# Optimization experiments

Measured on AMD Instinct MI355X. Metric: run time of the kernel, lower is better.

The kernel has to match this reference:

```python
import jax, jax.numpy as jnp
import numpy as np

# init config (from module __init__ / docstring example)
VOXEL_SIZE = np.array([0.2, 0.2, 8.0], dtype=np.float32)
PC_RANGE = np.array([0.0, -25.6, -3.0, 51.2, 25.6, 5.0], dtype=np.float32)
MAX_PTS = 32
MAX_VOX = 16000
GRID = (int((PC_RANGE[3] - PC_RANGE[0]) / VOXEL_SIZE[0]),
        int((PC_RANGE[4] - PC_RANGE[1]) / VOXEL_SIZE[1]),
        int((PC_RANGE[5] - PC_RANGE[2]) / VOXEL_SIZE[2]))  # (256, 256, 1)

N_POINTS = 4_000_000
C_FEAT = 4  # xyz + intensity


def setup_inputs() -> dict:
    key = jax.random.key(0)
    u = jax.random.uniform(key, (N_POINTS, C_FEAT), dtype=jnp.float32)
    lo = jnp.array([PC_RANGE[0], PC_RANGE[1], PC_RANGE[2], 0.0], jnp.float32)
    span = jnp.array([PC_RANGE[3] - PC_RANGE[0], PC_RANGE[4] - PC_RANGE[1],
                      PC_RANGE[5] - PC_RANGE[2], 1.0], jnp.float32)
    points = u * span + lo  # uniformly inside the point-cloud range
    return {"points": points}


def reference(points):
    """Hard voxelization. Returns fixed-size (padded) outputs:
    voxels [MAX_VOX, MAX_PTS, C], coords [MAX_VOX, 3] int32, num_points [MAX_VOX] int32.
    Unused voxel slots are zero (num_points==0), matching torch semantics up to padding."""
    N, C = points.shape
    Gx, Gy, Gz = GRID
    lo = jnp.asarray(PC_RANGE[:3])
    hi = jnp.asarray(PC_RANGE[3:])
    vsz = jnp.asarray(VOXEL_SIZE)

    xyz = points[:, :3]
    valid = jnp.all((xyz >= lo) & (xyz < hi), axis=1)  # in-range mask

    coords = jnp.floor((xyz - lo) / vsz).astype(jnp.int32)
    coords = jnp.clip(coords, 0, jnp.array([Gx - 1, Gy - 1, Gz - 1], jnp.int32))

    # linear voxel hash; invalid points get sentinel so they sort to the end
    BIG = Gx * Gy * Gz
    vhash = coords[:, 0] * (Gy * Gz) + coords[:, 1] * Gz + coords[:, 2]
    vhash = jnp.where(valid, vhash, BIG)

    order = jnp.argsort(vhash)
    sh = vhash[order]          # [N] sorted hashes
    sc = coords[order]         # [N,3]
    sp = points[order]         # [N,C]
    svalid = sh < BIG

    # segment boundaries of the sorted hash stream (== torch.unique inverse groups)
    newv = jnp.concatenate([jnp.array([True]), sh[1:] != sh[:-1]]) & svalid
    vid = jnp.cumsum(newv.astype(jnp.int32)) - 1   # voxel id per point (sorted order)

    idx = jnp.arange(N, dtype=jnp.int32)
    start = jax.lax.cummax(jnp.where(newv, idx, 0))  # index of first point of own voxel
    rank = idx - start                                # position within voxel

    keep = svalid & (rank < MAX_PTS) & (vid < MAX_VOX)
    vid_s = jnp.where(keep, vid, MAX_VOX)   # route dropped points to dump row
    rank_s = jnp.where(keep, rank, 0)

    voxels = jnp.zeros((MAX_VOX + 1, MAX_PTS, C), points.dtype)
    voxels = voxels.at[vid_s, rank_s].set(sp)[:MAX_VOX]

    cvid = jnp.where(newv & (vid < MAX_VOX), vid, MAX_VOX)
    coords_out = jnp.zeros((MAX_VOX + 1, 3), jnp.int32).at[cvid].set(sc)[:MAX_VOX]

    num_points = jax.ops.segment_sum(keep.astype(jnp.int32), vid_s,
                                     num_segments=MAX_VOX + 1)[:MAX_VOX]
    return voxels, coords_out, num_points
```

## Files before the change

### kernel.cpp

```cpp
#include <hip/hip_runtime.h>

#define NBINS    65536
#define NWORDS   16384
#define MAXVOX   16000
#define MAXPTS   32
#define NBLK     256
#define RSEG     8

#define COORDS_OFF (MAXVOX * MAXPTS * 4)
#define NP_OFF     (COORDS_OFF + MAXVOX * 3)

#define OFF_COUNTS   0u
#define OFF_STARTS   (256u << 10)
#define OFF_BINOF    (512u << 10)
#define OFF_PARTC    (576u << 10)
#define OFF_PARTO    (577u << 10)
#define OFF_VBIT     (640u << 10)
#define OFF_BINS16   (2u << 20)
#define OFF_PARTIAL  (10u << 20)
#define OFF_MEMBERS  (26u << 20)

__global__ __launch_bounds__(1024) void k_hist(const float4* __restrict__ pts, int n,
                                               unsigned short* __restrict__ bins16,
                                               unsigned long long* __restrict__ vbit,
                                               unsigned* __restrict__ partial) {
    __shared__ unsigned sh[NWORDS];
    int t = threadIdx.x, b = blockIdx.x;
    for (int w = t; w < NWORDS; w += 1024) sh[w] = 0u;
    __syncthreads();

    int chunk = (n + NBLK - 1) / NBLK;
    int s = b * chunk;
    int e = min(n, s + chunk);
    int k = 0;
    for (int i = s + t; i < e; i += 1024, ++k) {
        float4 p = pts[i];
        bool valid = (p.x >= 0.0f)   & (p.x < 51.2f) &
                     (p.y >= -25.6f) & (p.y < 25.6f) &
                     (p.z >= -3.0f)  & (p.z < 5.0f);
        int cx = (int)floorf((p.x - 0.0f)  / 0.2f);
        int cy = (int)floorf((p.y + 25.6f) / 0.2f);
        int cz = (int)floorf((p.z + 3.0f)  / 8.0f);
        cx = min(max(cx, 0), 255);
        cy = min(max(cy, 0), 255);
        cz = min(max(cz, 0), 0);
        unsigned bin = (unsigned)(cx * 256 + cy + cz);
        bins16[i] = (unsigned short)bin;
        unsigned long long mask = __ballot(valid);
        if ((t & 63) == 0) vbit[(size_t)b * 256 + (t >> 6) + k * 16] = mask;
        if (valid) atomicAdd(&sh[bin >> 2], 1u << ((bin & 3u) * 8u));
    }
    __syncthreads();
    unsigned* myp = partial + (size_t)b * NWORDS;
    for (int w = t; w < NWORDS; w += 1024) myp[w] = sh[w];
}

__global__ __launch_bounds__(512) void k_reduce(unsigned* __restrict__ partial,
                                                unsigned* __restrict__ counts,
                                                unsigned* __restrict__ partC,
                                                unsigned* __restrict__ partO,
                                                unsigned* __restrict__ binof) {
    __shared__ unsigned cache[NBLK][64];
    __shared__ unsigned segsum[RSEG][64][4];
    __shared__ unsigned red[512];
    int t = threadIdx.x;
    int g = blockIdx.x * 512 + t;
    if (g < MAXVOX) binof[g] = 0xFFFFFFFFu;

    int wl  = t & 63;
    int seg = t >> 6;
    int w   = blockIdx.x * 64 + wl;
    int blk0 = seg * (NBLK / RSEG);

    unsigned a0 = 0, a1 = 0, a2 = 0, a3 = 0;
    for (int b = 0; b < NBLK / RSEG; ++b) {
        unsigned v = partial[(size_t)(blk0 + b) * NWORDS + w];
        cache[blk0 + b][wl] = v;
        a0 += v & 255u; a1 += (v >> 8) & 255u;
        a2 += (v >> 16) & 255u; a3 += (v >> 24) & 255u;
    }
    segsum[seg][wl][0] = a0; segsum[seg][wl][1] = a1;
    segsum[seg][wl][2] = a2; segsum[seg][wl][3] = a3;
    __syncthreads();

    unsigned b0 = 0, b1 = 0, b2 = 0, b3 = 0;
    for (int s2 = 0; s2 < seg; ++s2) {
        b0 += segsum[s2][wl][0]; b1 += segsum[s2][wl][1];
        b2 += segsum[s2][wl][2]; b3 += segsum[s2][wl][3];
    }
    for (int b = 0; b < NBLK / RSEG; ++b) {
        unsigned v = cache[blk0 + b][wl];
        partial[(size_t)(blk0 + b) * NWORDS + w] =
            b0 | (b1 << 8) | (b2 << 16) | (b3 << 24);
        b0 += v & 255u; b1 += (v >> 8) & 255u;
        b2 += (v >> 16) & 255u; b3 += (v >> 24) & 255u;
    }

    unsigned mySum = 0, myOcc = 0;
    if (seg == RSEG - 1) {
        counts[w * 4 + 0] = b0; counts[w * 4 + 1] = b1;
        counts[w * 4 + 2] = b2; counts[w * 4 + 3] = b3;
        mySum = b0 + b1 + b2 + b3;
        myOcc = (b0 > 0u) + (b1 > 0u) + (b2 > 0u) + (b3 > 0u);
    }
    red[t] = mySum; __syncthreads();
    for (int off = 256; off > 0; off >>= 1) { if (t < off) red[t] += red[t + off]; __syncthreads(); }
    if (t == 0) partC[blockIdx.x] = red[0];
    __syncthreads();
    red[t] = myOcc; __syncthreads();
    for (int off = 256; off > 0; off >>= 1) { if (t < off) red[t] += red[t + off]; __syncthreads(); }
    if (t == 0) partO[blockIdx.x] = red[0];
}

__global__ __launch_bounds__(256) void k_scan3(const unsigned* __restrict__ counts,
                                               const unsigned* __restrict__ partC,
                                               const unsigned* __restrict__ partO,
                                               unsigned* __restrict__ starts,
                                               unsigned* __restrict__ binof,
                                               float* __restrict__ out) {
    __shared__ unsigned rc[256], ro[256], sc[256], so[256];
    int t = threadIdx.x;
    int bin = blockIdx.x * 256 + t;
    unsigned c = counts[bin];
    unsigned occ = (c > 0u) ? 1u : 0u;

    rc[t] = (t < blockIdx.x) ? partC[t] : 0u;
    ro[t] = (t < blockIdx.x) ? partO[t] : 0u;
    sc[t] = c; so[t] = occ;
    __syncthreads();
    for (int off = 128; off > 0; off >>= 1) {
        if (t < off) { rc[t] += rc[t + off]; ro[t] += ro[t + off]; }
        __syncthreads();
    }
    unsigned baseC = rc[0], baseO = ro[0];
    for (int off = 1; off < 256; off <<= 1) {
        unsigned ac = (t >= off) ? sc[t - off] : 0u;
        unsigned ao = (t >= off) ? so[t - off] : 0u;
        __syncthreads();
        sc[t] += ac; so[t] += ao;
        __syncthreads();
    }
    unsigned st  = baseC + (sc[t] - c);
    unsigned vid = baseO + (so[t] - occ);
    bool kept = occ && (vid < MAXVOX);
    starts[bin] = st | (kept ? 0u : 0x80000000u);
    if (kept) {
        binof[vid] = (unsigned)bin;
        out[COORDS_OFF + vid * 3 + 0] = (float)(bin >> 8);
        out[COORDS_OFF + vid * 3 + 1] = (float)(bin & 255);
        out[COORDS_OFF + vid * 3 + 2] = 0.0f;
        out[NP_OFF + vid] = (float)(c < MAXPTS ? c : MAXPTS);
    }
}

__global__ __launch_bounds__(1024) void k_scatter(const unsigned short* __restrict__ bins16,
                                                  const unsigned long long* __restrict__ vbit,
                                                  int n,
                                                  const unsigned* __restrict__ partial,
                                                  const unsigned* __restrict__ starts,
                                                  unsigned* __restrict__ members) {
    __shared__ unsigned sh[NWORDS];
    int t = threadIdx.x, b = blockIdx.x;
    const unsigned* myp = partial + (size_t)b * NWORDS;
    for (int w = t; w < NWORDS; w += 1024) sh[w] = myp[w];
    __syncthreads();

    int chunk = (n + NBLK - 1) / NBLK;
    int s = b * chunk;
    int e = min(n, s + chunk);
    int k = 0;
    for (int i = s + t; i < e; i += 1024, ++k) {
        unsigned long long mask = vbit[(size_t)b * 256 + (t >> 6) + k * 16];
        if ((mask >> (t & 63)) & 1ull) {
            unsigned v = (unsigned)bins16[i];
            unsigned st = starts[v];
            if (!(st & 0x80000000u)) {
                unsigned old = atomicAdd(&sh[v >> 2], 1u << ((v & 3u) * 8u));
                unsigned off = (old >> ((v & 3u) * 8u)) & 255u;
                members[st + off] = (unsigned)i;
            }
        }
    }
}

__global__ __launch_bounds__(256) void k_select(
        const unsigned* __restrict__ binof, const unsigned* __restrict__ counts,
        const unsigned* __restrict__ starts, const unsigned* __restrict__ members,
        const float4* __restrict__ pts, float* __restrict__ out) {
    float4* vox = (float4*)out;
    int v = blockIdx.x * 4 + (threadIdx.x >> 6);
    unsigned lane = threadIdx.x & 63u;
    const float4 z4 = {0.0f, 0.0f, 0.0f, 0.0f};
    unsigned bin = binof[v];
    if (bin == 0xFFFFFFFFu) {
        if (lane < 32u) vox[(size_t)v * MAXPTS + lane] = z4;
        if (lane < 3u)  out[COORDS_OFF + v * 3 + lane] = 0.0f;
        if (lane == 3u) out[NP_OFF + v] = 0.0f;
        return;
    }
    unsigned m  = counts[bin];
    unsigned mc = m > 64u ? 64u : m;
    unsigned np = m > 32u ? 32u : m;
    unsigned start = starts[bin] & 0x7FFFFFFFu;

    if (lane >= np && lane < 32u) vox[(size_t)v * MAXPTS + lane] = z4;

    unsigned e0 = (lane < mc) ? members[start + lane] : 0xFFFFFFFFu;
    unsigned r0 = 0;
    int jm = (int)mc;
    for (int j = 0; j < jm; ++j) {
        unsigned a0 = (unsigned)__shfl((int)e0, j);
        r0 += (a0 < e0);
    }
    if (e0 != 0xFFFFFFFFu && r0 < MAXPTS) vox[(size_t)v * MAXPTS + r0] = pts[e0];
}

extern "C" void kernel_launch(void* const* d_in, const int* in_sizes, int n_in,
                              void* d_out, int out_size, void* d_ws, size_t ws_size,
                              hipStream_t stream) {
    const float4* pts = (const float4*)d_in[0];
    int n = in_sizes[0] / 4;
    float* out = (float*)d_out;
    char* ws = (char*)d_ws;

    unsigned* counts  = (unsigned*)(ws + OFF_COUNTS);
    unsigned* starts  = (unsigned*)(ws + OFF_STARTS);
    unsigned* binof   = (unsigned*)(ws + OFF_BINOF);
    unsigned* partC   = (unsigned*)(ws + OFF_PARTC);
    unsigned* partO   = (unsigned*)(ws + OFF_PARTO);
    unsigned long long* vbit = (unsigned long long*)(ws + OFF_VBIT);
    unsigned short* bins16   = (unsigned short*)(ws + OFF_BINS16);
    unsigned* partial = (unsigned*)(ws + OFF_PARTIAL);
    unsigned* members = (unsigned*)(ws + OFF_MEMBERS);

    k_hist   <<<NBLK, 1024, 0, stream>>>(pts, n, bins16, vbit, partial);
    k_reduce <<<NWORDS / 64, 512, 0, stream>>>(partial, counts, partC, partO, binof);
    k_scan3  <<<256, 256, 0, stream>>>(counts, partC, partO, starts, binof, out);
    k_scatter<<<NBLK, 1024, 0, stream>>>(bins16, vbit, n, partial, starts, members);
    k_select <<<MAXVOX / 4, 256, 0, stream>>>(binof, counts, starts, members, pts, out);
}
```

Measured before the change: 75.97 us.

## Fuse scan kernel into reduce via decoupled inter-block prefix publication

Merges the separate scan kernel into the reduce kernel. Each block publishes its total count and occupancy to a global flag array with a release atomic store, then spins on the totals of all earlier blocks to form its base offsets. This removes one kernel launch and the global round trip of per-bin counts. In exchange it adds a spin-wait that assumes forward progress across the 256 co-resident blocks, plus extra block-wide reductions.

New measurement: 80.28 us. 5.7% more time.

```diff
diff --git a/kernel.cpp b/kernel.cpp
--- a/kernel.cpp
+++ b/kernel.cpp
@@ -13,8 +13,7 @@
 #define OFF_COUNTS   0u
 #define OFF_STARTS   (256u << 10)
 #define OFF_BINOF    (512u << 10)
-#define OFF_PARTC    (576u << 10)
-#define OFF_PARTO    (577u << 10)
+#define OFF_PUB      (576u << 10)
 #define OFF_VBIT     (640u << 10)
 #define OFF_BINS16   (2u << 20)
 #define OFF_PARTIAL  (10u << 20)
@@ -23,9 +22,11 @@
 __global__ __launch_bounds__(1024) void k_hist(const float4* __restrict__ pts, int n,
                                                unsigned short* __restrict__ bins16,
                                                unsigned long long* __restrict__ vbit,
-                                               unsigned* __restrict__ partial) {
+                                               unsigned* __restrict__ partial,
+                                               unsigned long long* __restrict__ pub) {
     __shared__ unsigned sh[NWORDS];
     int t = threadIdx.x, b = blockIdx.x;
+    if (b == 0 && t < 256) pub[t] = 0ull;
     for (int w = t; w < NWORDS; w += 1024) sh[w] = 0u;
     __syncthreads();
 
@@ -57,12 +58,15 @@
 
 __global__ __launch_bounds__(512) void k_reduce(unsigned* __restrict__ partial,
                                                 unsigned* __restrict__ counts,
-                                                unsigned* __restrict__ partC,
-                                                unsigned* __restrict__ partO,
-                                                unsigned* __restrict__ binof) {
+                                                unsigned long long* __restrict__ pub,
+                                                unsigned* __restrict__ starts,
+                                                unsigned* __restrict__ binof,
+                                                float* __restrict__ out) {
     __shared__ unsigned cache[NBLK][64];
     __shared__ unsigned segsum[RSEG][64][4];
     __shared__ unsigned red[512];
+    __shared__ unsigned cnt[256];
+    __shared__ unsigned sc[256], so[256];
     int t = threadIdx.x;
     int g = blockIdx.x * 512 + t;
     if (g < MAXVOX) binof[g] = 0xFFFFFFFFu;
@@ -100,56 +104,62 @@
     if (seg == RSEG - 1) {
         counts[w * 4 + 0] = b0; counts[w * 4 + 1] = b1;
         counts[w * 4 + 2] = b2; counts[w * 4 + 3] = b3;
+        cnt[wl * 4 + 0] = b0; cnt[wl * 4 + 1] = b1;
+        cnt[wl * 4 + 2] = b2; cnt[wl * 4 + 3] = b3;
         mySum = b0 + b1 + b2 + b3;
         myOcc = (b0 > 0u) + (b1 > 0u) + (b2 > 0u) + (b3 > 0u);
     }
     red[t] = mySum; __syncthreads();
     for (int off = 256; off > 0; off >>= 1) { if (t < off) red[t] += red[t + off]; __syncthreads(); }
-    if (t == 0) partC[blockIdx.x] = red[0];
-    __syncthreads();
+    unsigned localC = red[0]; __syncthreads();
     red[t] = myOcc; __syncthreads();
     for (int off = 256; off > 0; off >>= 1) { if (t < off) red[t] += red[t + off]; __syncthreads(); }
-    if (t == 0) partO[blockIdx.x] = red[0];
-}
-
-__global__ __launch_bounds__(256) void k_scan3(const unsigned* __restrict__ counts,
-                                               const unsigned* __restrict__ partC,
-                                               const unsigned* __restrict__ partO,
-                                               unsigned* __restrict__ starts,
-                                               unsigned* __restrict__ binof,
-                                               float* __restrict__ out) {
-    __shared__ unsigned rc[256], ro[256], sc[256], so[256];
-    int t = threadIdx.x;
-    int bin = blockIdx.x * 256 + t;
-    unsigned c = counts[bin];
-    unsigned occ = (c > 0u) ? 1u : 0u;
-
-    rc[t] = (t < blockIdx.x) ? partC[t] : 0u;
-    ro[t] = (t < blockIdx.x) ? partO[t] : 0u;
-    sc[t] = c; so[t] = occ;
-    __syncthreads();
-    for (int off = 128; off > 0; off >>= 1) {
-        if (t < off) { rc[t] += rc[t + off]; ro[t] += ro[t + off]; }
+    unsigned localO = red[0]; __syncthreads();
+
+    if (t == 0) {
+        unsigned long long val = (unsigned long long)localC |
+                                 ((unsigned long long)localO << 32) | (1ull << 63);
+        __hip_atomic_store(&pub[blockIdx.x], val, __ATOMIC_RELEASE, __HIP_MEMORY_SCOPE_AGENT);
+    }
+    unsigned long long myv = 0ull;
+    if (t < blockIdx.x) {
+        do {
+            myv = __hip_atomic_load(&pub[t], __ATOMIC_RELAXED, __HIP_MEMORY_SCOPE_AGENT);
+        } while (myv == 0ull);
+    }
+    red[t] = (unsigned)(myv & 0xFFFFFFFFull); __syncthreads();
+    for (int off = 256; off > 0; off >>= 1) { if (t < off) red[t] += red[t + off]; __syncthreads(); }
+    unsigned baseC = red[0]; __syncthreads();
+    red[t] = (unsigned)((myv >> 32) & 0x7FFFFFFFull); __syncthreads();
+    for (int off = 256; off > 0; off >>= 1) { if (t < off) red[t] += red[t + off]; __syncthreads(); }
+    unsigned baseO = red[0]; __syncthreads();
+
+    unsigned c = 0, occ = 0;
+    if (t < 256) {
+        c = cnt[t]; occ = (c > 0u) ? 1u : 0u;
+        sc[t] = c; so[t] = occ;
+    }
+    __syncthreads();
+    for (int off = 1; off < 256; off <<= 1) {
+        unsigned ac = 0, ao = 0;
+        if (t < 256 && t >= off) { ac = sc[t - off]; ao = so[t - off]; }
         __syncthreads();
-    }
-    unsigned baseC = rc[0], baseO = ro[0];
-    for (int off = 1; off < 256; off <<= 1) {
-        unsigned ac = (t >= off) ? sc[t - off] : 0u;
-        unsigned ao = (t >= off) ? so[t - off] : 0u;
+        if (t < 256) { sc[t] += ac; so[t] += ao; }
         __syncthreads();
-        sc[t] += ac; so[t] += ao;
-        __syncthreads();
-    }
-    unsigned st  = baseC + (sc[t] - c);
-    unsigned vid = baseO + (so[t] - occ);
-    bool kept = occ && (vid < MAXVOX);
-    starts[bin] = st | (kept ? 0u : 0x80000000u);
-    if (kept) {
-        binof[vid] = (unsigned)bin;
-        out[COORDS_OFF + vid * 3 + 0] = (float)(bin >> 8);
-        out[COORDS_OFF + vid * 3 + 1] = (float)(bin & 255);
-        out[COORDS_OFF + vid * 3 + 2] = 0.0f;
-        out[NP_OFF + vid] = (float)(c < MAXPTS ? c : MAXPTS);
+    }
+    if (t < 256) {
+        int bin = blockIdx.x * 256 + t;
+        unsigned st  = baseC + (sc[t] - c);
+        unsigned vid = baseO + (so[t] - occ);
+        bool kept = occ && (vid < MAXVOX);
+        starts[bin] = st | (kept ? 0u : 0x80000000u);
+        if (kept) {
+            binof[vid] = (unsigned)bin;
+            out[COORDS_OFF + vid * 3 + 0] = (float)(bin >> 8);
+            out[COORDS_OFF + vid * 3 + 1] = (float)(bin & 255);
+            out[COORDS_OFF + vid * 3 + 2] = 0.0f;
+            out[NP_OFF + vid] = (float)(c < MAXPTS ? c : MAXPTS);
+        }
     }
 }
 
@@ -226,16 +236,14 @@
     unsigned* counts  = (unsigned*)(ws + OFF_COUNTS);
     unsigned* starts  = (unsigned*)(ws + OFF_STARTS);
     unsigned* binof   = (unsigned*)(ws + OFF_BINOF);
-    unsigned* partC   = (unsigned*)(ws + OFF_PARTC);
-    unsigned* partO   = (unsigned*)(ws + OFF_PARTO);
+    unsigned long long* pub  = (unsigned long long*)(ws + OFF_PUB);
     unsigned long long* vbit = (unsigned long long*)(ws + OFF_VBIT);
     unsigned short* bins16   = (unsigned short*)(ws + OFF_BINS16);
     unsigned* partial = (unsigned*)(ws + OFF_PARTIAL);
     unsigned* members = (unsigned*)(ws + OFF_MEMBERS);
 
-    k_hist   <<<NBLK, 1024, 0, stream>>>(pts, n, bins16, vbit, partial);
-    k_reduce <<<NWORDS / 64, 512, 0, stream>>>(partial, counts, partC, partO, binof);
-    k_scan3  <<<256, 256, 0, stream>>>(counts, partC, partO, starts, binof, out);
+    k_hist   <<<NBLK, 1024, 0, stream>>>(pts, n, bins16, vbit, partial, pub);
+    k_reduce <<<NWORDS / 64, 512, 0, stream>>>(partial, counts, pub, starts, binof, out);
     k_scatter<<<NBLK, 1024, 0, stream>>>(bins16, vbit, n, partial, starts, members);
     k_select <<<MAXVOX / 4, 256, 0, stream>>>(binof, counts, starts, members, pts, out);
 }
```
